# Kernel optimization log

Hardware: AMD Instinct MI355X
Metric: run time of the kernel (lower is better)

The kernel has to match this reference:

```python
import jax, jax.numpy as jnp
import numpy as np

NUM_GRAPHS = 256
NEG_SLOPE = 0.2


def _gatv2(x, src, dst, Wl, Wr, att, bias, num_nodes):
    # GATv2Conv (heads=1): e_ij = att . leaky_relu(Wl x_j + Wr x_i), softmax over in-edges of i
    xl = x @ Wl  # [N, H] source transform
    xr = x @ Wr  # [N, H] target transform
    msg = xl[src]                      # [E, H]
    e = jax.nn.leaky_relu(msg + xr[dst], NEG_SLOPE) @ att  # [E]
    # segment softmax over destination node
    e_max = jax.ops.segment_max(e, dst, num_segments=num_nodes)
    e_exp = jnp.exp(e - e_max[dst])
    denom = jax.ops.segment_sum(e_exp, dst, num_segments=num_nodes)
    alpha = e_exp / denom[dst]         # [E]
    out = jax.ops.segment_sum(alpha[:, None] * msg, dst, num_segments=num_nodes)
    return out + bias


def setup_inputs() -> dict:
    key = jax.random.key(0)
    ks = jax.random.split(key, 16)
    N, E, D, H, O = 100000, 1600000, 64, 64, 64
    s = 0.05
    inp = {
        "x": jax.random.normal(ks[0], (N, D), dtype=jnp.float32),
        "edge_index": jax.random.randint(ks[1], (2, E), 0, N, dtype=jnp.int64),
        "batch": jnp.sort(jax.random.randint(ks[2], (N,), 0, NUM_GRAPHS, dtype=jnp.int64)),
        "W1l": jax.random.normal(ks[3], (D, H), dtype=jnp.float32) * s,
        "W1r": jax.random.normal(ks[4], (D, H), dtype=jnp.float32) * s,
        "att1": jax.random.normal(ks[5], (H,), dtype=jnp.float32) * s,
        "b1": jnp.zeros((H,), dtype=jnp.float32),
        "W2": jax.random.normal(ks[6], (H, H), dtype=jnp.float32) * s,
        "att2": jax.random.normal(ks[7], (H,), dtype=jnp.float32) * s,
        "b2": jnp.zeros((H,), dtype=jnp.float32),
        "W3": jax.random.normal(ks[8], (H, H), dtype=jnp.float32) * s,
        "att3": jax.random.normal(ks[9], (H,), dtype=jnp.float32) * s,
        "b3": jnp.zeros((H,), dtype=jnp.float32),
        "Wlin": jax.random.normal(ks[10], (H, O), dtype=jnp.float32) * s,
        "blin": jnp.zeros((O,), dtype=jnp.float32),
    }
    return inp


def reference(x, edge_index, batch, W1l, W1r, att1, b1, W2, att2, b2, W3, att3, b3, Wlin, blin):
    N = x.shape[0]
    # PyG GATv2Conv default add_self_loops=True
    loops = jnp.arange(N, dtype=edge_index.dtype)
    src = jnp.concatenate([edge_index[0], loops])
    dst = jnp.concatenate([edge_index[1], loops])

    h = jax.nn.relu(_gatv2(x, src, dst, W1l, W1r, att1, b1, N))
    h = jax.nn.relu(_gatv2(h, src, dst, W2, W2, att2, b2, N))  # share_weights=True
    h = _gatv2(h, src, dst, W3, W3, att3, b3, N)

    # global mean pool over graphs
    sums = jax.ops.segment_sum(h, batch, num_segments=NUM_GRAPHS)
    cnts = jax.ops.segment_sum(jnp.ones((N,), dtype=h.dtype), batch, num_segments=NUM_GRAPHS)
    pooled = sums / jnp.maximum(cnts, 1.0)[:, None]
    # dropout is identity in eval mode
    return pooled @ Wlin + blin
```

## Files before the change

kernel.cpp:

```cpp
#include <hip/hip_runtime.h>
#include <hip/hip_fp16.h>
#include <math.h>

#define NEG_SLOPE 0.2f
#define NUM_GRAPHS 256
#define LOG2E_F 1.44269504088896f

#define EPB   6656
#define EPT   13
#define BCAP  5120
#define MAXB  392

typedef _Float16 half8 __attribute__((ext_vector_type(8)));
typedef _Float16 f16x2 __attribute__((ext_vector_type(2)));
typedef float f32x4 __attribute__((ext_vector_type(4)));
typedef unsigned u32x2 __attribute__((ext_vector_type(2)));
typedef unsigned u32x4 __attribute__((ext_vector_type(4)));

__device__ __forceinline__ half8 bch8(uint4 u) { return __builtin_bit_cast(half8, u); }
__device__ __forceinline__ f16x2 bc2(unsigned u) { return __builtin_bit_cast(f16x2, u); }

__device__ __forceinline__ float hsum8_bcast(float x) {
    x += __int_as_float(__builtin_amdgcn_update_dpp(0, __float_as_int(x), 0x111, 0xF, 0xF, false));
    x += __int_as_float(__builtin_amdgcn_update_dpp(0, __float_as_int(x), 0x112, 0xF, 0xF, false));
    x += __int_as_float(__builtin_amdgcn_update_dpp(0, __float_as_int(x), 0x114, 0xF, 0xF, false));
    return __int_as_float(__builtin_amdgcn_ds_swizzle(__float_as_int(x), 0xF8));
}


__device__ __forceinline__ void bucketA_body(char* smem, int bid, int t,
                                             const int* __restrict__ src,
                                             const int* __restrict__ dst,
                                             unsigned* __restrict__ bucketFill,
                                             uint2* __restrict__ bucketArr,
                                             int E, int NBUCK) {
    uint2* sEdge = (uint2*)smem;
    unsigned* hist  = (unsigned*)(smem + EPB * 8);
    unsigned* lscan = hist + MAXB;
    unsigned* ebase = lscan + MAXB;
    unsigned* efill = ebase + MAXB;
    int e0 = bid * EPB;
    int cntE = E - e0; if (cntE > EPB) cntE = EPB;

    for (int b = t; b < MAXB; b += 512) { hist[b] = 0u; efill[b] = 0u; }
    __syncthreads();

    int es[EPT], ed[EPT];
#pragma unroll
    for (int k = 0; k < EPT; ++k) {
        int i = t + k * 512;
        bool v = i < cntE;
        es[k] = v ? __builtin_nontemporal_load(src + e0 + i) : 0;
        ed[k] = v ? __builtin_nontemporal_load(dst + e0 + i) : -1;
        if (v) atomicAdd(&hist[(unsigned)ed[k] >> 8], 1u);
    }
    __syncthreads();

    if (t < 64) {
        unsigned vals[7]; unsigned tot = 0u;
#pragma unroll
        for (int k = 0; k < 7; ++k) {
            int b = t * 7 + k;
            vals[k] = (b < MAXB) ? hist[b] : 0u;
            tot += vals[k];
        }
        unsigned sc = tot;
#pragma unroll
        for (int off = 1; off < 64; off <<= 1) {
            unsigned n = __shfl_up(sc, off, 64);
            if (t >= off) sc += n;
        }
        unsigned run = sc - tot;
#pragma unroll
        for (int k = 0; k < 7; ++k) {
            int b = t * 7 + k;
            if (b < MAXB) { lscan[b] = run; run += vals[k]; }
        }
    }
    __syncthreads();

    for (int b = t; b < NBUCK; b += 512) {
        unsigned c = hist[b];
        ebase[b] = c ? atomicAdd(&bucketFill[b], c) : 0u;
    }
    __syncthreads();

#pragma unroll
    for (int k = 0; k < EPT; ++k) {
        if (ed[k] >= 0) {
            unsigned b = (unsigned)ed[k] >> 8;
            unsigned p = lscan[b] + atomicAdd(&efill[b], 1u);
            sEdge[p] = make_uint2((unsigned)es[k], (unsigned)ed[k]);
        }
    }
    __syncthreads();

    for (int i = t; i < cntE; i += 512) {
        uint2 e = sEdge[i];
        unsigned b = e.y >> 8;
        unsigned pos = ebase[b] + ((unsigned)i - lscan[b]);
        if (pos < BCAP) bucketArr[(size_t)b * BCAP + pos] = e;
    }
}


__device__ __forceinline__ void stage_x32_row(const float* __restrict__ X, _Float16* sXp,
                                              int r0, int lr, int c0, int N) {
    int row = r0 + lr;
    f32x4 x0 = {0.f,0.f,0.f,0.f}, x1 = x0, x2 = x0, x3 = x0;
    if (row < N) {
        const f32x4* Xv = (const f32x4*)(X + (size_t)row * 64 + c0);
        x0 = __builtin_nontemporal_load(Xv);
        x1 = __builtin_nontemporal_load(Xv + 1);
        x2 = __builtin_nontemporal_load(Xv + 2);
        x3 = __builtin_nontemporal_load(Xv + 3);
    }
    __half2 hh[8] = {
        __floats2half2_rn(x0[0], x0[1]), __floats2half2_rn(x0[2], x0[3]),
        __floats2half2_rn(x1[0], x1[1]), __floats2half2_rn(x1[2], x1[3]),
        __floats2half2_rn(x2[0], x2[1]), __floats2half2_rn(x2[2], x2[3]),
        __floats2half2_rn(x3[0], x3[1]), __floats2half2_rn(x3[2], x3[3])};
    *(uint4*)(sXp + lr * 72 + c0)     = ((uint4*)hh)[0];
    *(uint4*)(sXp + lr * 72 + c0 + 8) = ((uint4*)hh)[1];
}

__device__ __forceinline__ void stage_x16(const __half* __restrict__ X, _Float16* sXp,
                                          int r0, int t, int N) {
    int lr = t >> 2, c0 = (t & 3) * 16;
    int row = r0 + lr;
    uint4 u0 = make_uint4(0u,0u,0u,0u), u1 = u0;
    if (row < N) {
        const uint4* Xv = (const uint4*)(X + (size_t)row * 64 + c0);
        u0 = Xv[0]; u1 = Xv[1];
    }
    *(uint4*)(sXp + lr * 72 + c0)     = u0;
    *(uint4*)(sXp + lr * 72 + c0 + 8) = u1;
}

__device__ __forceinline__ void stage_wt(const float* __restrict__ W, _Float16* sWt, int t) {
    int k = t >> 2, nq = (t & 3) * 16;
    const float4* wr = (const float4*)(W + k * 64 + nq);
    float4 w0 = wr[0], w1 = wr[1], w2 = wr[2], w3 = wr[3];
    float ws[16] = {w0.x, w0.y, w0.z, w0.w, w1.x, w1.y, w1.z, w1.w,
                    w2.x, w2.y, w2.z, w2.w, w3.x, w3.y, w3.z, w3.w};
#pragma unroll
    for (int i = 0; i < 16; ++i)
        sWt[(nq + i) * 72 + k] = (_Float16)ws[i];
}

__device__ __forceinline__ void stage_wt512(const float* __restrict__ W, _Float16* sWt, int t) {
    int k = t >> 3, nq = (t & 7) * 8;
    const float4* wr = (const float4*)(W + k * 64 + nq);
    float4 w0 = wr[0], w1 = wr[1];
    float ws[8] = {w0.x, w0.y, w0.z, w0.w, w1.x, w1.y, w1.z, w1.w};
#pragma unroll
    for (int i = 0; i < 8; ++i)
        sWt[(nq + i) * 72 + k] = (_Float16)ws[i];
}

__device__ __forceinline__ void mfma_tile(const _Float16* sXp, const _Float16* sWt,
                                          int m0, int lane, f32x4 acc[4]) {
    int lrow = lane & 15, hi = lane >> 4;
    uint4 ua0 = *(const uint4*)(sXp + (m0 + lrow) * 72 + hi * 8);
    uint4 ua1 = *(const uint4*)(sXp + (m0 + lrow) * 72 + 32 + hi * 8);
    half8 a0 = bch8(ua0), a1 = bch8(ua1);
#pragma unroll
    for (int nt = 0; nt < 4; ++nt) {
        uint4 ub0 = *(const uint4*)(sWt + (nt * 16 + lrow) * 72 + hi * 8);
        uint4 ub1 = *(const uint4*)(sWt + (nt * 16 + lrow) * 72 + 32 + hi * 8);
        acc[nt] = __builtin_amdgcn_mfma_f32_16x16x32_f16(a0, bch8(ub0), acc[nt], 0, 0, 0);
        acc[nt] = __builtin_amdgcn_mfma_f32_16x16x32_f16(a1, bch8(ub1), acc[nt], 0, 0, 0);
    }
}

__device__ __forceinline__ void mfma_store_co(const f32x4 acc[4], __half* Y16,
                                              _Float16* srow, int r0, int m0,
                                              int lane, int N) {
    int lrow = lane & 15, hi = lane >> 4;
#pragma unroll
    for (int nt = 0; nt < 4; ++nt)
#pragma unroll
        for (int r = 0; r < 4; ++r)
            srow[(hi * 4 + r) * 72 + nt * 16 + lrow] = (_Float16)acc[nt][r];
    __syncthreads();
    int row = lane >> 3, c8 = (lane & 7) * 8;
#pragma unroll
    for (int i = 0; i < 2; ++i) {
        int m = r0 + m0 + row + i * 8;
        uint4 v = *(const uint4*)(srow + (row + i * 8) * 72 + c8);
        if (m < N) *(uint4*)(Y16 + (size_t)m * 64 + c8) = v;
    }
}

__global__ __launch_bounds__(512) void k_gemm1_bucketA(
        const float* __restrict__ X, const float* __restrict__ Wl, const float* __restrict__ Wr,
        __half* __restrict__ Yl16, __half* __restrict__ Yr16, int N,
        const int* __restrict__ src, const int* __restrict__ dst,
        unsigned* __restrict__ bucketFill, uint2* __restrict__ bucketArr,
        int E, int NBUCK, int aBlocks, int g1Blocks,
        const float* __restrict__ att1, const float* __restrict__ att2,
        const float* __restrict__ att3, __half* __restrict__ att16) {
    __shared__ uint4 smemq[3720];
    char* smem = (char*)smemq;
    int bid = blockIdx.x;
    int t = threadIdx.x;
    if (bid < aBlocks) {
        bucketA_body(smem, bid, t, src, dst, bucketFill, bucketArr, E, NBUCK);
        return;
    }
    if (bid >= aBlocks + g1Blocks) {
        if (t < 192) {
            int layer = t >> 6, f = t & 63;
            const float* ap = (layer == 0) ? att1 : (layer == 1) ? att2 : att3;
            att16[layer * 64 + f] = __float2half(ap[f] * LOG2E_F);
        }
        return;
    }
    _Float16* sXp  = (_Float16*)smem;
    _Float16* sWtl = sXp + 128 * 72;
    _Float16* sWtr = sWtl + 64 * 72;
    _Float16* srep = sWtr + 64 * 72;
    int r0 = (bid - aBlocks) * 128;
    stage_x32_row(X, sXp, r0, t >> 2, (t & 3) * 16, N);
    stage_wt512(Wl, sWtl, t);
    stage_wt512(Wr, sWtr, t);
    __syncthreads();
    int lane = t & 63;
    int m0 = (t >> 6) * 16;
    _Float16* srow = srep + (t >> 6) * 16 * 72;
    f32x4 accl[4] = {}, accr[4] = {};
    mfma_tile(sXp, sWtl, m0, lane, accl);
    mfma_tile(sXp, sWtr, m0, lane, accr);
    mfma_store_co(accl, Yl16, srow, r0, m0, lane, N);
    mfma_store_co(accr, Yr16, srow, r0, m0, lane, N);
}

__global__ __launch_bounds__(512) void k_bucketB(const uint2* __restrict__ bucketArr,
                                                 const unsigned* __restrict__ bucketFill,
                                                 int* __restrict__ cnt, int* __restrict__ csrF,
                                                 const int* __restrict__ batch,
                                                 int* __restrict__ gstart,
                                                 int N, int E) {
    __shared__ int stage[256 * 64];
    __shared__ unsigned h[256];
    int t = threadIdx.x;
    int b = blockIdx.x;
    int n0 = b << 8;
    if (t < 256) h[t] = 1u;
    {
        uint4* sz = (uint4*)stage;
#pragma unroll
        for (int k = 0; k < 8; ++k) sz[t + k * 512] = make_uint4(0u, 0u, 0u, 0u);
    }
    __syncthreads();
    if (t < 256) stage[t << 6] = n0 + t;
    __syncthreads();

    unsigned ec = bucketFill[b]; if (ec > BCAP) ec = BCAP;
    for (unsigned i = t; i < ec; i += 512) {
        uint2 e = bucketArr[(size_t)b * BCAP + i];
        unsigned v = e.y & 255u;
        unsigned r = atomicAdd(&h[v], 1u);
        if (r < 64u) {
            unsigned pos = (r < 32u) ? (((r & 7u) << 2) + (r >> 3))
                                     : (32u + ((r & 7u) << 2) + ((r >> 3) - 4u));
            stage[(v << 6) + pos] = (int)e.x;
        }
    }
    __syncthreads();

    int node = n0 + t;
    if (t < 256 && node < N) {
        unsigned d = h[t];
        cnt[node] = (int)(d < 64u ? d : 64u);
        int bb = batch[node];
        if (node == 0) {
            for (int g = 0; g <= bb; ++g) gstart[g] = 0;
        } else {
            int pb = batch[node - 1];
            for (int g = pb + 1; g <= bb; ++g) gstart[g] = node;
        }
        if (node == N - 1) {
            for (int g = bb + 1; g <= NUM_GRAPHS; ++g) gstart[g] = N;
        }
    }

    int nrows = N - n0; if (nrows > 256) nrows = 256;
    int total4 = nrows << 4;
    uint4* d4 = (uint4*)(csrF + ((size_t)n0 << 6));
    const uint4* s4 = (const uint4*)stage;
    for (int k = t; k < total4; k += 512) d4[k] = s4[k];
}

__global__ __launch_bounds__(256) void k_gemm_l2(const __half* __restrict__ X,
                                                 const float* __restrict__ W,
                                                 __half* __restrict__ Y16, int N) {
    __shared__ _Float16 s[128 * 72 + 64 * 72 + 4 * 16 * 72];
    _Float16* sXp = s;
    _Float16* sWt = s + 128 * 72;
    _Float16* srep = sWt + 64 * 72;
    int t = threadIdx.x;
    int r0 = blockIdx.x * 128;
    stage_x16(X, sXp, r0, t, N);
    stage_x16(X, sXp + 64 * 72, r0 + 64, t, N);
    stage_wt(W, sWt, t);
    __syncthreads();
    int lane = t & 63;
    int w = t >> 6;
    _Float16* srow = srep + w * 16 * 72;
#pragma unroll
    for (int half_ = 0; half_ < 2; ++half_) {
        int m0 = half_ * 64 + w * 16;
        f32x4 acc[4] = {};
        mfma_tile(sXp, sWt, m0, lane, acc);
        mfma_store_co(acc, Y16, srow, r0, m0, lane, N);
    }
}


#define AGG_STEP(P, K)                                                       \
    { half8 v_ = bch8(P);                                                    \
      half8 t_ = v_ + X8;                                                    \
      t_ = __builtin_elementwise_max(t_, t_ * (_Float16)NEG_SLOPE);          \
      uint4 tu_ = __builtin_bit_cast(uint4, t_);                             \
      float sc_ = __builtin_amdgcn_fdot2(bc2(ua.x), bc2(tu_.x), 0.f, false); \
      sc_ = __builtin_amdgcn_fdot2(bc2(ua.y), bc2(tu_.y), sc_, false);       \
      sc_ = __builtin_amdgcn_fdot2(bc2(ua.z), bc2(tu_.z), sc_, false);       \
      sc_ = __builtin_amdgcn_fdot2(bc2(ua.w), bc2(tu_.w), sc_, false);       \
      sc_ = hsum8_bcast(sc_);                                                \
      float w_ = ((K) * 8 + s < degs) ? exp2f(sc_) : 0.f;                    \
      l_acc += w_;                                                           \
      _Pragma("unroll") for (int j_ = 0; j_ < 8; ++j_)                       \
          acc[j_] = fmaf((float)v_[j_], w_, acc[j_]);                        \
    }

__global__ void k_agg8(const __half* __restrict__ xl, const __half* __restrict__ xrh,
                       const __half* __restrict__ att16, const float* __restrict__ bias,
                       const int* __restrict__ cnt, const int* __restrict__ csrF,
                       __half* __restrict__ out16, int N, int do_relu) {
    int wid = (blockIdx.x * blockDim.x + threadIdx.x) >> 6;
    if (wid >= N) return;
    int lane = threadIdx.x & 63;
    int q = lane & 7, s = lane >> 3;
    int fb = q * 8;

    int degs = __builtin_amdgcn_readfirstlane(cnt[wid]);
    const int* crow = csrF + ((size_t)wid << 6);

    u32x4 idxv = __builtin_nontemporal_load((const u32x4*)(crow + s * 4));
    uint4 ux = *(const uint4*)(xrh + ((size_t)wid << 6) + fb);
    uint4 ua = *(const uint4*)(att16 + fb);

    uint4 pA = *(const uint4*)(xl + ((size_t)idxv[0] << 6) + fb);
    uint4 pB = *(const uint4*)(xl + ((size_t)idxv[1] << 6) + fb);
    uint4 pC = *(const uint4*)(xl + ((size_t)idxv[2] << 6) + fb);
    uint4 pD = *(const uint4*)(xl + ((size_t)idxv[3] << 6) + fb);

    half8 X8 = bch8(ux);
    float l_acc = 0.f;
    float acc[8];
#pragma unroll
    for (int j = 0; j < 8; ++j) acc[j] = 0.f;

    AGG_STEP(pA, 0);
    if (degs > 8)  AGG_STEP(pB, 1);
    if (degs > 16) AGG_STEP(pC, 2);
    if (degs > 24) {
        AGG_STEP(pD, 3);
        if (degs > 32) {
            u32x4 idx2 = __builtin_nontemporal_load((const u32x4*)(crow + 32 + s * 4));
            uint4 qA = *(const uint4*)(xl + ((size_t)idx2[0] << 6) + fb);
            uint4 qB = *(const uint4*)(xl + ((size_t)idx2[1] << 6) + fb);
            uint4 qC = *(const uint4*)(xl + ((size_t)idx2[2] << 6) + fb);
            uint4 qD = *(const uint4*)(xl + ((size_t)idx2[3] << 6) + fb);
            AGG_STEP(qA, 4);
            if (degs > 40) AGG_STEP(qB, 5);
            if (degs > 48) AGG_STEP(qC, 6);
            if (degs > 56) AGG_STEP(qD, 7);
        }
    }

    l_acc += __shfl_xor(l_acc, 8, 64);
#pragma unroll
    for (int j = 0; j < 8; ++j) acc[j] += __shfl_xor(acc[j], 8, 64);
    int par = s & 1;
    float b0 = par ? acc[4] : acc[0];
    float b1 = par ? acc[5] : acc[1];
    float b2 = par ? acc[6] : acc[2];
    float b3 = par ? acc[7] : acc[3];
#pragma unroll
    for (int o = 16; o <= 32; o <<= 1) {
        l_acc += __shfl_xor(l_acc, o, 64);
        b0 += __shfl_xor(b0, o, 64);
        b1 += __shfl_xor(b1, o, 64);
        b2 += __shfl_xor(b2, o, 64);
        b3 += __shfl_xor(b3, o, 64);
    }

    if (s < 2) {
        float rl = 1.0f / l_acc;
        int fo = fb + s * 4;
        float4 bv = *(const float4*)(bias + fo);
        float a0 = b0 * rl + bv.x;
        float a1 = b1 * rl + bv.y;
        float a2 = b2 * rl + bv.z;
        float a3 = b3 * rl + bv.w;
        if (do_relu) {
            a0 = fmaxf(a0, 0.f); a1 = fmaxf(a1, 0.f);
            a2 = fmaxf(a2, 0.f); a3 = fmaxf(a3, 0.f);
        }
        __half2 h0 = __floats2half2_rn(a0, a1);
        __half2 h1 = __floats2half2_rn(a2, a3);
        uint2 u;
        u.x = __builtin_bit_cast(unsigned, h0);
        u.y = __builtin_bit_cast(unsigned, h1);
        *(uint2*)(out16 + (size_t)wid * 64 + fo) = u;
    }
}


__global__ __launch_bounds__(256) void k_pool_final(const __half* __restrict__ h16,
                                                    const int* __restrict__ gstart,
                                                    const float* __restrict__ Wlin,
                                                    const float* __restrict__ blin,
                                                    float* __restrict__ out) {
    __shared__ float red[4][64];
    int g = blockIdx.x;
    int t = threadIdx.x;
    int w = t >> 6, lane = t & 63;
    int i0 = gstart[g], i1 = gstart[g + 1];
    const unsigned* hu = (const unsigned*)h16;
    int half_ = lane >> 5;
    int u = lane & 31;
    float sx = 0.f, sy = 0.f;
    for (int i = i0 + w * 2 + half_; i < i1; i += 8) {
        unsigned v = __builtin_nontemporal_load(hu + (size_t)i * 32 + u);
        float2 p = __half22float2(__builtin_bit_cast(__half2, v));
        sx += p.x; sy += p.y;
    }
    sx += __shfl_xor(sx, 32, 64);
    sy += __shfl_xor(sy, 32, 64);
    if (lane < 32) { red[w][2 * u] = sx; red[w][2 * u + 1] = sy; }
    __syncthreads();
    if (w == 0) {
        float s = red[0][lane] + red[1][lane] + red[2][lane] + red[3][lane];
        float cden = (float)((i1 - i0) > 1 ? (i1 - i0) : 1);
        float pld = s / cden;
        float acc = blin[lane];
        for (int k = 0; k < 64; ++k) {
            acc += __shfl(pld, k, 64) * Wlin[k * 64 + lane];
        }
        out[g * 64 + lane] = acc;
    }
}


extern "C" void kernel_launch(void* const* d_in, const int* in_sizes, int n_in,
                              void* d_out, int out_size, void* d_ws, size_t ws_size,
                              hipStream_t stream) {
    const float* x    = (const float*)d_in[0];
    const int*   ei   = (const int*)d_in[1];
    const int*   batch= (const int*)d_in[2];
    const float* W1l  = (const float*)d_in[3];
    const float* W1r  = (const float*)d_in[4];
    const float* att1 = (const float*)d_in[5];
    const float* b1   = (const float*)d_in[6];
    const float* W2   = (const float*)d_in[7];
    const float* att2 = (const float*)d_in[8];
    const float* b2   = (const float*)d_in[9];
    const float* W3   = (const float*)d_in[10];
    const float* att3 = (const float*)d_in[11];
    const float* b3   = (const float*)d_in[12];
    const float* Wlin = (const float*)d_in[13];
    const float* blin = (const float*)d_in[14];

    const int N = in_sizes[0] / 64;
    const int E = in_sizes[1] / 2;
    const int* src = ei;
    const int* dst = ei + E;
    const int NBUCK = (N + 255) >> 8;

    char* p = (char*)d_ws;
    auto alloc = [&](size_t bytes) -> void* {
        void* r = (void*)p;
        p += (bytes + 255) & ~(size_t)255;
        return r;
    };
    float*  bufB32 = (float*)alloc((size_t)N * 64 * 4);
    __half* buf16  = (__half*)alloc((size_t)N * 64 * 2);
    __half* bufC16 = (__half*)alloc((size_t)N * 64 * 2);
    int*    csrF   = (int*)alloc((size_t)N * 64 * 4);
    int*    cnt    = (int*)alloc((size_t)N * 4);
    int*    gstart = (int*)alloc((size_t)(NUM_GRAPHS + 1) * 4);
    __half* att16  = (__half*)alloc((size_t)3 * 64 * 2);
    uint2*    bucketArr  = (uint2*)bufB32;
    unsigned* bucketFill = (unsigned*)((char*)bufB32 + ((size_t)20 << 20));

    const int B = 256;
    const int gemmBlocks = (N + 127) >> 7;
    const int aggBlocks = ((size_t)N * 64 + B - 1) / B;
    const int aBlocks = (E + EPB - 1) / EPB;
    const int g1Blocks = (N + 127) >> 7;

    hipMemsetAsync(bucketFill, 0, (size_t)NBUCK * 4, stream);
    k_gemm1_bucketA<<<aBlocks + g1Blocks + 1, 512, 0, stream>>>(
        x, W1l, W1r, buf16, bufC16, N, src, dst, bucketFill, bucketArr,
        E, NBUCK, aBlocks, g1Blocks, att1, att2, att3, att16);
    k_bucketB<<<NBUCK, 512, 0, stream>>>(bucketArr, bucketFill, cnt, csrF, batch, gstart, N, E);

    k_agg8<<<aggBlocks, B, 0, stream>>>(buf16, bufC16, att16, b1, cnt, csrF,
                                        bufC16, N, 1);
    k_gemm_l2<<<gemmBlocks, B, 0, stream>>>(bufC16, W2, buf16, N);
    k_agg8<<<aggBlocks, B, 0, stream>>>(buf16, buf16, att16 + 64, b2, cnt, csrF,
                                        bufC16, N, 1);
    k_gemm_l2<<<gemmBlocks, B, 0, stream>>>(bufC16, W3, buf16, N);
    k_agg8<<<aggBlocks, B, 0, stream>>>(buf16, buf16, att16 + 128, b3, cnt, csrF,
                                        bufC16, N, 0);

    k_pool_final<<<NUM_GRAPHS, B, 0, stream>>>(bufC16, gstart, Wlin, blin, (float*)d_out);
}
```

Baseline: 300.5 us.

## Drop nontemporal loads and shrink layer-2/3 GEMM blocks to 64 rows

Replaces nontemporal loads with ordinary cached loads in edge bucketing, x staging and pooling. Also halves the rows per block in the layer-2/3 GEMM from 128 to 64, which doubles the grid and reduces LDS per block. This looks like a partial rollback of an earlier round of micro-optimisations. The GEMM is small relative to aggregation, so the overall effect is likely small either way.

After: 288.7 us. -3.9%, faster.

```diff
diff --git a/kernel.cpp b/kernel.cpp
--- a/kernel.cpp
+++ b/kernel.cpp
@@ -14,7 +14,6 @@
 typedef _Float16 half8 __attribute__((ext_vector_type(8)));
 typedef _Float16 f16x2 __attribute__((ext_vector_type(2)));
 typedef float f32x4 __attribute__((ext_vector_type(4)));
-typedef unsigned u32x2 __attribute__((ext_vector_type(2)));
 typedef unsigned u32x4 __attribute__((ext_vector_type(4)));
 
 __device__ __forceinline__ half8 bch8(uint4 u) { return __builtin_bit_cast(half8, u); }
@@ -50,8 +49,8 @@
     for (int k = 0; k < EPT; ++k) {
         int i = t + k * 512;
         bool v = i < cntE;
-        es[k] = v ? __builtin_nontemporal_load(src + e0 + i) : 0;
-        ed[k] = v ? __builtin_nontemporal_load(dst + e0 + i) : -1;
+        es[k] = v ? src[e0 + i] : 0;
+        ed[k] = v ? dst[e0 + i] : -1;
         if (v) atomicAdd(&hist[(unsigned)ed[k] >> 8], 1u);
     }
     __syncthreads();
@@ -107,19 +106,18 @@
 __device__ __forceinline__ void stage_x32_row(const float* __restrict__ X, _Float16* sXp,
                                               int r0, int lr, int c0, int N) {
     int row = r0 + lr;
-    f32x4 x0 = {0.f,0.f,0.f,0.f}, x1 = x0, x2 = x0, x3 = x0;
+    float4 x0, x1, x2, x3;
     if (row < N) {
-        const f32x4* Xv = (const f32x4*)(X + (size_t)row * 64 + c0);
-        x0 = __builtin_nontemporal_load(Xv);
-        x1 = __builtin_nontemporal_load(Xv + 1);
-        x2 = __builtin_nontemporal_load(Xv + 2);
-        x3 = __builtin_nontemporal_load(Xv + 3);
+        const float4* Xv = (const float4*)(X + (size_t)row * 64 + c0);
+        x0 = Xv[0]; x1 = Xv[1]; x2 = Xv[2]; x3 = Xv[3];
+    } else {
+        x0 = x1 = x2 = x3 = make_float4(0.f, 0.f, 0.f, 0.f);
     }
     __half2 hh[8] = {
-        __floats2half2_rn(x0[0], x0[1]), __floats2half2_rn(x0[2], x0[3]),
-        __floats2half2_rn(x1[0], x1[1]), __floats2half2_rn(x1[2], x1[3]),
-        __floats2half2_rn(x2[0], x2[1]), __floats2half2_rn(x2[2], x2[3]),
-        __floats2half2_rn(x3[0], x3[1]), __floats2half2_rn(x3[2], x3[3])};
+        __floats2half2_rn(x0.x, x0.y), __floats2half2_rn(x0.z, x0.w),
+        __floats2half2_rn(x1.x, x1.y), __floats2half2_rn(x1.z, x1.w),
+        __floats2half2_rn(x2.x, x2.y), __floats2half2_rn(x2.z, x2.w),
+        __floats2half2_rn(x3.x, x3.y), __floats2half2_rn(x3.z, x3.w)};
     *(uint4*)(sXp + lr * 72 + c0)     = ((uint4*)hh)[0];
     *(uint4*)(sXp + lr * 72 + c0 + 8) = ((uint4*)hh)[1];
 }
@@ -295,26 +293,21 @@
 __global__ __launch_bounds__(256) void k_gemm_l2(const __half* __restrict__ X,
                                                  const float* __restrict__ W,
                                                  __half* __restrict__ Y16, int N) {
-    __shared__ _Float16 s[128 * 72 + 64 * 72 + 4 * 16 * 72];
+    __shared__ _Float16 s[64 * 72 + 64 * 72 + 4 * 16 * 72];
     _Float16* sXp = s;
-    _Float16* sWt = s + 128 * 72;
+    _Float16* sWt = s + 64 * 72;
     _Float16* srep = sWt + 64 * 72;
     int t = threadIdx.x;
-    int r0 = blockIdx.x * 128;
+    int r0 = blockIdx.x * 64;
     stage_x16(X, sXp, r0, t, N);
-    stage_x16(X, sXp + 64 * 72, r0 + 64, t, N);
     stage_wt(W, sWt, t);
     __syncthreads();
     int lane = t & 63;
-    int w = t >> 6;
-    _Float16* srow = srep + w * 16 * 72;
-#pragma unroll
-    for (int half_ = 0; half_ < 2; ++half_) {
-        int m0 = half_ * 64 + w * 16;
-        f32x4 acc[4] = {};
-        mfma_tile(sXp, sWt, m0, lane, acc);
-        mfma_store_co(acc, Y16, srow, r0, m0, lane, N);
-    }
+    int m0 = (t >> 6) * 16;
+    _Float16* srow = srep + (t >> 6) * 16 * 72;
+    f32x4 acc[4] = {};
+    mfma_tile(sXp, sWt, m0, lane, acc);
+    mfma_store_co(acc, Y16, srow, r0, m0, lane, N);
 }
 
 
@@ -434,7 +427,7 @@
     int u = lane & 31;
     float sx = 0.f, sy = 0.f;
     for (int i = i0 + w * 2 + half_; i < i1; i += 8) {
-        unsigned v = __builtin_nontemporal_load(hu + (size_t)i * 32 + u);
+        unsigned v = hu[(size_t)i * 32 + u];
         float2 p = __half22float2(__builtin_bit_cast(__half2, v));
         sx += p.x; sy += p.y;
     }
@@ -497,7 +490,7 @@
     unsigned* bucketFill = (unsigned*)((char*)bufB32 + ((size_t)20 << 20));
 
     const int B = 256;
-    const int gemmBlocks = (N + 127) >> 7;
+    const int gemmBlocks = (N + 63) / 64;
     const int aggBlocks = ((size_t)N * 64 + B - 1) / B;
     const int aBlocks = (E + EPB - 1) / EPB;
     const int g1Blocks = (N + 127) >> 7;
```
